# Performance work log

Hardware: AMD Instinct MI355X
Metric: run time of the kernel (lower is better)

## Reference

```python
import jax, jax.numpy as jnp
import numpy as np

EPS = 1e-12  # torch F.normalize default eps


def _l2norm(x):
    n = jnp.sqrt(jnp.sum(x * x, axis=-1, keepdims=True))
    return x / jnp.maximum(n, EPS)


def setup_inputs() -> dict:
    key = jax.random.key(0)
    ks = jax.random.split(key, 8)
    B, T, V = 4, 2048, 512
    C, H, NB = 512, 4, 64
    return {
        "x": jax.random.normal(ks[0], (B, T, V), dtype=jnp.float32),
        "basis": jax.random.normal(ks[1], (V, 2 * NB), dtype=jnp.float32),
        "shared_q_w": jax.random.normal(ks[2], (V, C), dtype=jnp.float32) * 0.02,
        "shared_k_w": jax.random.normal(ks[3], (V, C), dtype=jnp.float32) * 0.02,
        "v_coeffs": jax.random.normal(ks[4], (C, 2 * NB), dtype=jnp.float32) * 0.02,
        "o_coeffs": jax.random.normal(ks[5], (C, 2 * NB), dtype=jnp.float32) * 0.02,
        "decay_logits": jnp.linspace(1.0, 5.0, H, dtype=jnp.float32),
        "out_scale": jnp.float32(0.1),
    }


def reference(x, basis, shared_q_w, shared_k_w, v_coeffs, o_coeffs, decay_logits, out_scale):
    B, T, V = x.shape
    H = decay_logits.shape[0]
    C = shared_q_w.shape[1]
    D = C // H

    v_w = basis @ v_coeffs.T  # [V, C]
    o_w = basis @ o_coeffs.T  # [V, C]

    q = _l2norm(x @ shared_q_w)  # [B, T, C]
    k = _l2norm(x @ shared_k_w)
    v = x @ v_w

    # [B, H, T, D]
    q = q.reshape(B, T, H, D).transpose(0, 2, 1, 3)
    k = k.reshape(B, T, H, D).transpose(0, 2, 1, 3)
    v = v.reshape(B, T, H, D).transpose(0, 2, 1, 3)

    scores = jnp.einsum("bhqd,bhkd->bhqk", q, k)  # [B, H, T, T]

    decay = jax.nn.sigmoid(decay_logits)  # [H]
    pos = jnp.arange(T)
    diff = pos[None, :] - pos[:, None]  # diff[i, j] = j - i
    mask = (diff > 0).astype(scores.dtype)  # [T, T]
    expo = jnp.clip(diff.astype(jnp.float32) - 1.0, 0.0, None)  # [T, T]
    decay_w = (decay[:, None, None] ** expo[None]) * mask[None]  # [H, T, T]

    scores = scores * decay_w[None].astype(scores.dtype)
    retrieved = jnp.einsum("bhqk,bhkd->bhqd", scores, v)  # [B, H, T, D]
    retrieved = retrieved.transpose(0, 2, 1, 3).reshape(B, T, C)
    return retrieved @ o_w.T * out_scale  # [B, T, V]
```

## Files before the change

### kernel.cpp

```cpp
#include <hip/hip_runtime.h>
#include <hip/hip_bf16.h>

#define BB 4
#define TT 2048
#define VV 512
#define CC 512
#define HH 4
#define DD 128
#define NB2 128
#define NROWS (BB*TT)
#define QC 64
#define NCH (TT/QC)
#define SST 66
#define EPS 1e-12f

typedef __attribute__((ext_vector_type(8))) short bf16x8;
typedef __attribute__((ext_vector_type(4))) float f32x4;
typedef unsigned short u16;

__device__ __forceinline__ void gl_lds16(const void* g, void* l) {
    __builtin_amdgcn_global_load_lds(
        (const __attribute__((address_space(1))) unsigned int*)g,
        (__attribute__((address_space(3))) unsigned int*)l, 16, 0, 0);
}
__device__ __forceinline__ u16 f2bu(float x) {
    __hip_bfloat16 h = __float2bfloat16(x);
    return *reinterpret_cast<u16*>(&h);
}
__device__ __forceinline__ float bu2f(u16 u) {
    __hip_bfloat16 h = *reinterpret_cast<__hip_bfloat16*>(&u);
    return __bfloat162float(h);
}

#define PREP_CVT   4096
#define PREP_TR    512
#define PREP_CB    64
#define PREP_Z     16
__global__ __launch_bounds__(256) void prep_all(
    const float* __restrict__ x, const float* __restrict__ qw,
    const float* __restrict__ kw, const float* __restrict__ basis,
    const float* __restrict__ v_coeffs, const float* __restrict__ o_coeffs,
    const float* __restrict__ out_scale,
    u16* __restrict__ xb, u16* __restrict__ wq, u16* __restrict__ wk,
    u16* __restrict__ bab, u16* __restrict__ vcb, u16* __restrict__ ocb,
    float* __restrict__ norms)
{
    __shared__ float tile[32][33];
    const int bi = blockIdx.x, t = threadIdx.x;
    if (bi < PREP_CVT) {
        int i = bi * 256 + t;
        float4 v = ((const float4*)x)[i];
        u16 h[4] = {f2bu(v.x), f2bu(v.y), f2bu(v.z), f2bu(v.w)};
        ((uint2*)xb)[i] = *(uint2*)h;
    } else if (bi < PREP_CVT + PREP_TR) {
        int id = bi - PREP_CVT;
        const int z = id >> 8; id &= 255;
        const float* in = z ? kw : qw;
        u16* outT = z ? wk : wq;
        const int bx = (id & 15) * 32, by = (id >> 4) * 32;
        const int tx = t & 31, ty = t >> 5;
        #pragma unroll
        for (int r = 0; r < 32; r += 8)
            tile[ty + r][tx] = in[(size_t)(by + ty + r) * CC + bx + tx];
        __syncthreads();
        #pragma unroll
        for (int r = 0; r < 32; r += 8)
            outT[(size_t)(bx + ty + r) * VV + by + tx] = f2bu(tile[tx][ty + r]);
    } else if (bi < PREP_CVT + PREP_TR + 3 * PREP_CB) {
        int id = bi - PREP_CVT - PREP_TR;
        const int which = id / PREP_CB;
        int i = (id - which * PREP_CB) * 256 + t;
        const float* src = which == 0 ? basis : (which == 1 ? v_coeffs : o_coeffs);
        u16* dst = which == 0 ? bab : (which == 1 ? vcb : ocb);
        const float sc = which == 2 ? out_scale[0] : 1.f;
        float4 v = ((const float4*)src)[i];
        u16 h[4] = {f2bu(v.x * sc), f2bu(v.y * sc), f2bu(v.z * sc), f2bu(v.w * sc)};
        ((uint2*)dst)[i] = *(uint2*)h;
    } else {
        int idx = (bi - PREP_CVT - PREP_TR - 3 * PREP_CB) * 256 + t;
        ((float4*)norms)[idx] = make_float4(0.f, 0.f, 0.f, 0.f);
    }
}

template <bool BF16OUT, bool NORMS>
__device__ __forceinline__ void gemm_body(
    const u16* __restrict__ A, const u16* __restrict__ Bt,
    void* __restrict__ Cp, int M, int N, int K, int m0, int n0,
    u16* __restrict__ As, u16* __restrict__ Bs, float* __restrict__ normp)
{
    const int t = threadIdx.x;
    const int wave = t >> 6, lane = t & 63;
    const int qq = lane >> 4, l16 = lane & 15;
    const int wm = (wave >> 1) * 64, wn = (wave & 1) * 64;

    const int s0 = wave * 128 + lane, s1 = s0 + 64;
    const int r0_ = s0 >> 2, c0_ = ((s0 & 3) - (r0_ >> 1)) & 3;
    const int r1_ = s1 >> 2, c1_ = ((s1 & 3) - (r1_ >> 1)) & 3;
    const u16* ga0 = A  + (size_t)(m0 + r0_) * K + c0_ * 8;
    const u16* ga1 = A  + (size_t)(m0 + r1_) * K + c1_ * 8;
    const u16* gb0 = Bt + (size_t)(n0 + r0_) * K + c0_ * 8;
    const u16* gb1 = Bt + (size_t)(n0 + r1_) * K + c1_ * 8;
    const int lo0 = (wave * 128) * 8, lo1 = (wave * 128 + 64) * 8;

    gl_lds16(ga0, As + lo0);
    gl_lds16(ga1, As + lo1);
    gl_lds16(gb0, Bs + lo0);
    gl_lds16(gb1, Bs + lo1);

    f32x4 acc[4][4];
    #pragma unroll
    for (int i = 0; i < 4; ++i)
        #pragma unroll
        for (int j = 0; j < 4; ++j) acc[i][j] = (f32x4){0.f, 0.f, 0.f, 0.f};

    int ib = 0;
    for (int k0 = 0; k0 < K; k0 += 32, ib ^= 1) {
        __syncthreads();
        if (k0 + 32 < K) {
            const int off = (ib ^ 1) * 4096;
            gl_lds16(ga0 + k0 + 32, As + off + lo0);
            gl_lds16(ga1 + k0 + 32, As + off + lo1);
            gl_lds16(gb0 + k0 + 32, Bs + off + lo0);
            gl_lds16(gb1 + k0 + 32, Bs + off + lo1);
        }
        const u16* Ac = As + ib * 4096;
        const u16* Bc = Bs + ib * 4096;
        bf16x8 af[4], bfr[4];
        #pragma unroll
        for (int mt = 0; mt < 4; ++mt) {
            const int r = wm + mt * 16 + l16;
            af[mt] = *(const bf16x8*)&Ac[(r * 4 + ((qq + (r >> 1)) & 3)) * 8];
        }
        #pragma unroll
        for (int nt = 0; nt < 4; ++nt) {
            const int r = wn + nt * 16 + l16;
            bfr[nt] = *(const bf16x8*)&Bc[(r * 4 + ((qq + (r >> 1)) & 3)) * 8];
        }
        #pragma unroll
        for (int mt = 0; mt < 4; ++mt)
            #pragma unroll
            for (int nt = 0; nt < 4; ++nt)
                acc[mt][nt] = __builtin_amdgcn_mfma_f32_16x16x32_bf16(
                    af[mt], bfr[nt], acc[mt][nt], 0, 0, 0);
    }
    #pragma unroll
    for (int mt = 0; mt < 4; ++mt)
        #pragma unroll
        for (int r = 0; r < 4; ++r) {
            int grow = m0 + wm + mt * 16 + qq * 4 + r;
            #pragma unroll
            for (int nt = 0; nt < 4; ++nt) {
                int gcol = n0 + wn + nt * 16 + l16;
                if (BF16OUT)
                    ((u16*)Cp)[(size_t)grow * N + gcol] = f2bu(acc[mt][nt][r]);
                else
                    ((float*)Cp)[(size_t)grow * N + gcol] = acc[mt][nt][r];
            }
        }
    if (NORMS && normp) {
        #pragma unroll
        for (int mt = 0; mt < 4; ++mt)
            #pragma unroll
            for (int r = 0; r < 4; ++r) {
                float s = 0.f;
                #pragma unroll
                for (int nt = 0; nt < 4; ++nt) {
                    float v = acc[mt][nt][r];
                    s = fmaf(v, v, s);
                }
                s += __shfl_xor(s, 1, 64);
                s += __shfl_xor(s, 2, 64);
                s += __shfl_xor(s, 4, 64);
                s += __shfl_xor(s, 8, 64);
                if (l16 == 0)
                    atomicAdd(&normp[m0 + wm + mt * 16 + qq * 4 + r], s);
            }
    }
}

__global__ __launch_bounds__(256) void gemm_w(
    const u16* __restrict__ bab, const u16* __restrict__ vcb,
    const u16* __restrict__ ocb, u16* __restrict__ v_wT, u16* __restrict__ o_ws)
{
    __shared__ __align__(16) u16 As[8192];
    __shared__ __align__(16) u16 Bs[8192];
    const int sec = blockIdx.x >> 2;
    const u16* A  = sec ? bab : vcb;
    const u16* Bt = sec ? ocb : bab;
    u16* C = sec ? o_ws : v_wT;
    gemm_body<true, false>(A, Bt, C, 512, 512, NB2,
                           blockIdx.y * 128, (blockIdx.x & 3) * 128, As, Bs, nullptr);
}

__global__ __launch_bounds__(256) void gemm_qkv(
    const u16* __restrict__ xb, const u16* __restrict__ wcat,
    u16* __restrict__ qo, u16* __restrict__ ko, u16* __restrict__ vo,
    float* __restrict__ norms)
{
    __shared__ __align__(16) u16 As[8192];
    __shared__ __align__(16) u16 Bs[8192];
    const int sec = blockIdx.x >> 2;
    u16* outp = sec == 0 ? qo : (sec == 1 ? ko : vo);
    float* np = sec == 0 ? norms : (sec == 1 ? norms + NROWS : nullptr);
    gemm_body<true, true>(xb, wcat + (size_t)sec * VV * CC, outp,
                          NROWS, CC, VV, blockIdx.y * 128, (blockIdx.x & 3) * 128,
                          As, Bs, np);
}

__global__ __launch_bounds__(256) void gemm_out(
    const u16* __restrict__ Ab, const u16* __restrict__ Btb, float* __restrict__ C)
{
    __shared__ __align__(16) u16 As[8192];
    __shared__ __align__(16) u16 Bs[8192];
    gemm_body<false, false>(Ab, Btb, C, NROWS, VV, CC,
                            blockIdx.y * 128, blockIdx.x * 128, As, Bs, nullptr);
}

__global__ __launch_bounds__(256) void state_local(
    const u16* __restrict__ kb, const u16* __restrict__ vb,
    const float* __restrict__ norms_k, const float* __restrict__ dlog,
    u16* __restrict__ statesb)
{
    __shared__ float ksA[16][132];
    __shared__ float vsA[16][132];
    const int c  = blockIdx.x;
    const int bh = blockIdx.y;
    const int b = bh >> 2, h = bh & 3;
    const float lam = 1.f / (1.f + __expf(-dlog[h]));
    const float l2lam = log2f(lam);
    const int t = threadIdx.x;
    const int tx = t & 15, ty = t >> 4;
    const int row0 = b * TT + c * QC;
    const size_t gbase = (size_t)row0 * CC + h * DD;

    float acc[8][8] = {};

    for (int j0 = 0; j0 < QC; j0 += 16) {
        __syncthreads();
        {
            const int r = t >> 4, c8 = (t & 15) * 8;
            uint4 kraw = *(const uint4*)(kb + gbase + (size_t)(j0 + r) * CC + c8);
            uint4 vraw = *(const uint4*)(vb + gbase + (size_t)(j0 + r) * CC + c8);
            const u16* kp = (const u16*)&kraw;
            const u16* vp = (const u16*)&vraw;
            const float w = exp2f((float)(j0 + r) * l2lam);
            const float rk = 1.f / fmaxf(sqrtf(norms_k[row0 + j0 + r]), EPS);
            *(float4*)&ksA[r][c8]     = make_float4(bu2f(kp[0]) * rk, bu2f(kp[1]) * rk, bu2f(kp[2]) * rk, bu2f(kp[3]) * rk);
            *(float4*)&ksA[r][c8 + 4] = make_float4(bu2f(kp[4]) * rk, bu2f(kp[5]) * rk, bu2f(kp[6]) * rk, bu2f(kp[7]) * rk);
            *(float4*)&vsA[r][c8]     = make_float4(bu2f(vp[0]) * w, bu2f(vp[1]) * w, bu2f(vp[2]) * w, bu2f(vp[3]) * w);
            *(float4*)&vsA[r][c8 + 4] = make_float4(bu2f(vp[4]) * w, bu2f(vp[5]) * w, bu2f(vp[6]) * w, bu2f(vp[7]) * w);
        }
        __syncthreads();
        #pragma unroll
        for (int jj = 0; jj < 16; ++jj) {
            float4 va0 = *(const float4*)&vsA[jj][ty * 8];
            float4 va1 = *(const float4*)&vsA[jj][ty * 8 + 4];
            float4 ka0 = *(const float4*)&ksA[jj][tx * 8];
            float4 ka1 = *(const float4*)&ksA[jj][tx * 8 + 4];
            float vd[8] = {va0.x, va0.y, va0.z, va0.w, va1.x, va1.y, va1.z, va1.w};
            float ke[8] = {ka0.x, ka0.y, ka0.z, ka0.w, ka1.x, ka1.y, ka1.z, ka1.w};
            #pragma unroll
            for (int a = 0; a < 8; ++a)
                #pragma unroll
                for (int d = 0; d < 8; ++d)
                    acc[a][d] = fmaf(vd[a], ke[d], acc[a][d]);
        }
    }
    u16* so = statesb + ((size_t)(bh * NCH + c) << 14);
    #pragma unroll
    for (int a = 0; a < 8; ++a) {
        u16 h8[8];
        #pragma unroll
        for (int d = 0; d < 8; ++d) h8[d] = f2bu(acc[a][d]);
        *(uint4*)(so + (size_t)(ty * 8 + a) * DD + tx * 8) = *(uint4*)h8;
    }
}

__global__ __launch_bounds__(256) void state_combine(
    const float* __restrict__ dlog, u16* __restrict__ statesb)
{
    const int bh = blockIdx.x >> 3, part = blockIdx.x & 7;
    const int h = bh & 3;
    const float lam = 1.f / (1.f + __expf(-dlog[h]));
    const float lamQ = exp2f((float)QC * log2f(lam));
    const int t = threadIdx.x;
    float run[8] = {};
    uint4* pbase = (uint4*)(statesb + ((size_t)(bh * NCH) << 14)) + part * 256 + t;
    uint4 cur = pbase[(size_t)(NCH - 1) * 2048];
    for (int c = NCH - 1; c >= 0; --c) {
        uint4 nxt = cur;
        if (c) nxt = pbase[(size_t)(c - 1) * 2048];
        u16* hb = (u16*)&cur;
        uint4 outw;
        u16* ho = (u16*)&outw;
        #pragma unroll
        for (int i = 0; i < 8; ++i) {
            float tmp = bu2f(hb[i]);
            ho[i] = f2bu(run[i]);
            run[i] = fmaf(lamQ, run[i], tmp);
        }
        pbase[(size_t)c * 2048] = outw;
        cur = nxt;
    }
}

__global__ __launch_bounds__(256) void attention_fused(
    const u16* __restrict__ qb, const u16* __restrict__ kb,
    const u16* __restrict__ vb, const u16* __restrict__ statesb,
    const float* __restrict__ norms, const float* __restrict__ dlog,
    u16* __restrict__ retb)
{
    __shared__ __align__(16) u16 qs[QC][DD];
    __shared__ __align__(16) u16 ks[QC][DD];
    __shared__ __align__(16) u16 vsT[DD][SST];
    __shared__ __align__(16) u16 ss[QC][SST];
    __shared__ float rql[QC], rkl[QC];

    const int c = blockIdx.x, bh = blockIdx.y;
    const int b = bh >> 2, h = bh & 3;
    const float lam = 1.f / (1.f + __expf(-dlog[h]));
    const float l2lam = log2f(lam);
    const int t = threadIdx.x;
    const int row0 = b * TT + c * QC;
    const size_t base = (size_t)row0 * CC + h * DD;

    const int wave = t >> 6, lane = t & 63;
    const int quad = lane >> 4, l16 = lane & 15;
    const int r0 = wave * 16;

    {
        const int lrow = lane >> 4;
        const int lcol = (lane & 15) * 8;
        #pragma unroll
        for (int u = 0; u < 4; ++u) {
            const int r = wave * 16 + u * 4;
            gl_lds16(qb + base + (size_t)(r + lrow) * CC + lcol, &qs[r][0]);
            gl_lds16(kb + base + (size_t)(r + lrow) * CC + lcol, &ks[r][0]);
        }
    }
    if (t < QC)            rql[t]      = 1.f / fmaxf(sqrtf(norms[row0 + t]), EPS);
    else if (t < 2 * QC)   rkl[t - QC] = 1.f / fmaxf(sqrtf(norms[NROWS + row0 + t - QC]), EPS);
    {
        const int j2 = t & 31, d0 = (t >> 5) * 16;
        const u16* v0 = vb + base + (size_t)(2 * j2) * CC + d0;
        const u16* v1 = v0 + CC;
        uint4 a0 = *(const uint4*)v0;
        uint4 a1 = *(const uint4*)(v0 + 8);
        uint4 b0 = *(const uint4*)v1;
        uint4 b1 = *(const uint4*)(v1 + 8);
        const u16* ap0 = (const u16*)&a0; const u16* ap1 = (const u16*)&a1;
        const u16* bp0 = (const u16*)&b0; const u16* bp1 = (const u16*)&b1;
        #pragma unroll
        for (int i = 0; i < 8; ++i) {
            *(unsigned int*)&vsT[d0 + i][2 * j2] =
                (unsigned int)ap0[i] | ((unsigned int)bp0[i] << 16);
            *(unsigned int*)&vsT[d0 + 8 + i][2 * j2] =
                (unsigned int)ap1[i] | ((unsigned int)bp1[i] << 16);
        }
    }
    __syncthreads();

    bf16x8 aq[4];
    #pragma unroll
    for (int kq = 0; kq < 4; ++kq)
        aq[kq] = *(const bf16x8*)&qs[r0 + l16][kq * 32 + quad * 8];

    f32x4 accs[4];
    #pragma unroll
    for (int nt = 0; nt < 4; ++nt) accs[nt] = (f32x4){0.f, 0.f, 0.f, 0.f};
    #pragma unroll
    for (int nt = 0; nt < 4; ++nt)
        #pragma unroll
        for (int kq = 0; kq < 4; ++kq) {
            bf16x8 bk = *(const bf16x8*)&ks[nt * 16 + l16][kq * 32 + quad * 8];
            accs[nt] = __builtin_amdgcn_mfma_f32_16x16x32_bf16(aq[kq], bk, accs[nt], 0, 0, 0);
        }

    #pragma unroll
    for (int nt = 0; nt < 4; ++nt) {
        const int j = nt * 16 + l16;
        const float rkj = rkl[j];
        #pragma unroll
        for (int rr = 0; rr < 4; ++rr) {
            const int i = r0 + quad * 4 + rr;
            const int di = j - i;
            float p = (di > 0) ? accs[nt][rr] * exp2f((float)(di - 1) * l2lam) * rkj : 0.f;
            ss[i][j] = f2bu(p);
        }
    }

    const u16* sb = statesb + ((size_t)(bh * NCH + c) << 14);
    f32x4 accc[8];
    #pragma unroll
    for (int nt = 0; nt < 8; ++nt) accc[nt] = (f32x4){0.f, 0.f, 0.f, 0.f};
    #pragma unroll
    for (int nt = 0; nt < 8; ++nt)
        #pragma unroll
        for (int kq = 0; kq < 4; ++kq) {
            bf16x8 bs_ = *(const bf16x8*)(sb + (size_t)(nt * 16 + l16) * DD + kq * 32 + quad * 8);
            accc[nt] = __builtin_amdgcn_mfma_f32_16x16x32_bf16(aq[kq], bs_, accc[nt], 0, 0, 0);
        }

    bf16x8 ap[2];
    #pragma unroll
    for (int kj = 0; kj < 2; ++kj)
        ap[kj] = *(const bf16x8*)&ss[r0 + l16][kj * 32 + quad * 8];
    f32x4 accd[8];
    #pragma unroll
    for (int nt = 0; nt < 8; ++nt) accd[nt] = (f32x4){0.f, 0.f, 0.f, 0.f};
    #pragma unroll
    for (int nt = 0; nt < 8; ++nt)
        #pragma unroll
        for (int kj = 0; kj < 2; ++kj) {
            bf16x8 bv = *(const bf16x8*)&vsT[nt * 16 + l16][kj * 32 + quad * 8];
            accd[nt] = __builtin_amdgcn_mfma_f32_16x16x32_bf16(ap[kj], bv, accd[nt], 0, 0, 0);
        }

    u16* rb = retb + (size_t)row0 * CC + h * DD;
    #pragma unroll
    for (int rr = 0; rr < 4; ++rr) {
        const int ii = r0 + quad * 4 + rr;
        const float wrow = exp2f((float)(QC - 1 - ii) * l2lam);
        const float rq = rql[ii];
        #pragma unroll
        for (int nt = 0; nt < 8; ++nt) {
            float val = (accd[nt][rr] + wrow * accc[nt][rr]) * rq;
            rb[(size_t)ii * CC + nt * 16 + l16] = f2bu(val);
        }
    }
}

extern "C" void kernel_launch(void* const* d_in, const int* in_sizes, int n_in,
                              void* d_out, int out_size, void* d_ws, size_t ws_size,
                              hipStream_t stream) {
    const float* x         = (const float*)d_in[0];
    const float* basis     = (const float*)d_in[1];
    const float* qw        = (const float*)d_in[2];
    const float* kw        = (const float*)d_in[3];
    const float* v_coeffs  = (const float*)d_in[4];
    const float* o_coeffs  = (const float*)d_in[5];
    const float* dlog      = (const float*)d_in[6];
    const float* out_scale = (const float*)d_in[7];
    float* out             = (float*)d_out;

    u16* p = (u16*)d_ws;
    u16* qb      = p;
    u16* kb      = qb + (size_t)NROWS * CC;
    u16* vb      = kb + (size_t)NROWS * CC;
    u16* statesb = vb + (size_t)NROWS * CC;
    u16* xb      = statesb + (size_t)BB * HH * NCH * DD * DD;
    u16* retb    = xb;
    u16* wcat    = xb + (size_t)NROWS * CC;
    u16* o_ws    = wcat + 3 * (size_t)VV * CC;
    float* norms = (float*)(o_ws + (size_t)VV * CC);
    u16* bab     = (u16*)(norms + 2 * NROWS);
    u16* vcb     = bab + (size_t)VV * NB2;
    u16* ocb     = vcb + (size_t)VV * NB2;

    prep_all<<<PREP_CVT + PREP_TR + 3 * PREP_CB + PREP_Z, 256, 0, stream>>>(
        x, qw, kw, basis, v_coeffs, o_coeffs, out_scale,
        xb, wcat, wcat + (size_t)VV * CC, bab, vcb, ocb, norms);
    gemm_w<<<dim3(8, 4), 256, 0, stream>>>(bab, vcb, ocb,
                                           wcat + 2 * (size_t)VV * CC, o_ws);
    gemm_qkv<<<dim3(12, NROWS / 128), 256, 0, stream>>>(xb, wcat, qb, kb, vb, norms);
    state_local  <<<dim3(NCH, BB * HH), 256, 0, stream>>>(kb, vb, norms + NROWS,
                                                          dlog, statesb);
    state_combine<<<BB * HH * 8, 256, 0, stream>>>(dlog, statesb);
    attention_fused<<<dim3(NCH, BB * HH), 256, 0, stream>>>(qb, kb, vb, statesb,
                                                            norms, dlog, retb);
    gemm_out<<<dim3(CC / 128, NROWS / 128), 256, 0, stream>>>(retb, o_ws, out);
}
```

Before: 181.6 us.

## Use MFMA for chunk states, swizzle LDS in attention, shrink output GEMM tiles

The chunk-state kernel moves from scalar fp32 outer-product FMAs to bf16 MFMA over transposed K/V tiles in LDS, which adds bf16 rounding of the scaled inputs. The attention kernel now loads its state matrix through swizzled LDS reused from the Q/K buffer rather than reading it directly from global memory, and adds barriers to make that reuse safe. The output GEMM gets a dedicated 64x128 tile kernel, doubling the block count to improve occupancy across CUs. These changes target the scalar-compute bottleneck in state_local and the poorly-coalesced global state reads.

```diff
diff --git a/kernel.cpp b/kernel.cpp
--- a/kernel.cpp
+++ b/kernel.cpp
@@ -207,13 +207,75 @@
                           As, Bs, np);
 }
 
-__global__ __launch_bounds__(256) void gemm_out(
-    const u16* __restrict__ Ab, const u16* __restrict__ Btb, float* __restrict__ C)
-{
-    __shared__ __align__(16) u16 As[8192];
+__global__ __launch_bounds__(256) void gemm_out64(
+    const u16* __restrict__ A, const u16* __restrict__ Bt, float* __restrict__ C)
+{
+    __shared__ __align__(16) u16 As[4096];
     __shared__ __align__(16) u16 Bs[8192];
-    gemm_body<false, false>(Ab, Btb, C, NROWS, VV, CC,
-                            blockIdx.y * 128, blockIdx.x * 128, As, Bs, nullptr);
+    const int t = threadIdx.x;
+    const int wave = t >> 6, lane = t & 63;
+    const int qq = lane >> 4, l16 = lane & 15;
+    const int m0 = blockIdx.y * 64, n0 = blockIdx.x * 128;
+    const int wm = (wave >> 1) * 32, wn = (wave & 1) * 64;
+    const int N = VV, K = CC;
+
+    const int sA = wave * 64 + lane;
+    const int rA = sA >> 2, cA = ((sA & 3) - (rA >> 1)) & 3;
+    const int sB0 = wave * 128 + lane, sB1 = sB0 + 64;
+    const int rB0 = sB0 >> 2, cB0 = ((sB0 & 3) - (rB0 >> 1)) & 3;
+    const int rB1 = sB1 >> 2, cB1 = ((sB1 & 3) - (rB1 >> 1)) & 3;
+    const u16* ga  = A  + (size_t)(m0 + rA) * K + cA * 8;
+    const u16* gb0 = Bt + (size_t)(n0 + rB0) * K + cB0 * 8;
+    const u16* gb1 = Bt + (size_t)(n0 + rB1) * K + cB1 * 8;
+    const int loA = wave * 512, loB0 = wave * 1024, loB1 = wave * 1024 + 512;
+
+    gl_lds16(ga, As + loA);
+    gl_lds16(gb0, Bs + loB0);
+    gl_lds16(gb1, Bs + loB1);
+
+    f32x4 acc[2][4];
+    #pragma unroll
+    for (int i = 0; i < 2; ++i)
+        #pragma unroll
+        for (int j = 0; j < 4; ++j) acc[i][j] = (f32x4){0.f, 0.f, 0.f, 0.f};
+
+    int ib = 0;
+    for (int k0 = 0; k0 < K; k0 += 32, ib ^= 1) {
+        __syncthreads();
+        if (k0 + 32 < K) {
+            gl_lds16(ga + k0 + 32,  As + (ib ^ 1) * 2048 + loA);
+            gl_lds16(gb0 + k0 + 32, Bs + (ib ^ 1) * 4096 + loB0);
+            gl_lds16(gb1 + k0 + 32, Bs + (ib ^ 1) * 4096 + loB1);
+        }
+        const u16* Ac = As + ib * 2048;
+        const u16* Bc = Bs + ib * 4096;
+        bf16x8 af[2], bfr[4];
+        #pragma unroll
+        for (int mt = 0; mt < 2; ++mt) {
+            const int r = wm + mt * 16 + l16;
+            af[mt] = *(const bf16x8*)&Ac[(r * 4 + ((qq + (r >> 1)) & 3)) * 8];
+        }
+        #pragma unroll
+        for (int nt = 0; nt < 4; ++nt) {
+            const int r = wn + nt * 16 + l16;
+            bfr[nt] = *(const bf16x8*)&Bc[(r * 4 + ((qq + (r >> 1)) & 3)) * 8];
+        }
+        #pragma unroll
+        for (int mt = 0; mt < 2; ++mt)
+            #pragma unroll
+            for (int nt = 0; nt < 4; ++nt)
+                acc[mt][nt] = __builtin_amdgcn_mfma_f32_16x16x32_bf16(
+                    af[mt], bfr[nt], acc[mt][nt], 0, 0, 0);
+    }
+    #pragma unroll
+    for (int mt = 0; mt < 2; ++mt)
+        #pragma unroll
+        for (int r = 0; r < 4; ++r) {
+            int grow = m0 + wm + mt * 16 + qq * 4 + r;
+            #pragma unroll
+            for (int nt = 0; nt < 4; ++nt)
+                C[(size_t)grow * N + n0 + wn + nt * 16 + l16] = acc[mt][nt][r];
+        }
 }
 
 __global__ __launch_bounds__(256) void state_local(
@@ -221,59 +283,77 @@
     const float* __restrict__ norms_k, const float* __restrict__ dlog,
     u16* __restrict__ statesb)
 {
-    __shared__ float ksA[16][132];
-    __shared__ float vsA[16][132];
-    const int c  = blockIdx.x;
-    const int bh = blockIdx.y;
+    __shared__ __align__(16) u16 vT[DD][SST];
+    __shared__ __align__(16) u16 kT[DD][SST];
+    const int c = blockIdx.x, bh = blockIdx.y;
     const int b = bh >> 2, h = bh & 3;
     const float lam = 1.f / (1.f + __expf(-dlog[h]));
     const float l2lam = log2f(lam);
     const int t = threadIdx.x;
-    const int tx = t & 15, ty = t >> 4;
     const int row0 = b * TT + c * QC;
     const size_t gbase = (size_t)row0 * CC + h * DD;
 
-    float acc[8][8] = {};
-
-    for (int j0 = 0; j0 < QC; j0 += 16) {
-        __syncthreads();
-        {
-            const int r = t >> 4, c8 = (t & 15) * 8;
-            uint4 kraw = *(const uint4*)(kb + gbase + (size_t)(j0 + r) * CC + c8);
-            uint4 vraw = *(const uint4*)(vb + gbase + (size_t)(j0 + r) * CC + c8);
-            const u16* kp = (const u16*)&kraw;
-            const u16* vp = (const u16*)&vraw;
-            const float w = exp2f((float)(j0 + r) * l2lam);
-            const float rk = 1.f / fmaxf(sqrtf(norms_k[row0 + j0 + r]), EPS);
-            *(float4*)&ksA[r][c8]     = make_float4(bu2f(kp[0]) * rk, bu2f(kp[1]) * rk, bu2f(kp[2]) * rk, bu2f(kp[3]) * rk);
-            *(float4*)&ksA[r][c8 + 4] = make_float4(bu2f(kp[4]) * rk, bu2f(kp[5]) * rk, bu2f(kp[6]) * rk, bu2f(kp[7]) * rk);
-            *(float4*)&vsA[r][c8]     = make_float4(bu2f(vp[0]) * w, bu2f(vp[1]) * w, bu2f(vp[2]) * w, bu2f(vp[3]) * w);
-            *(float4*)&vsA[r][c8 + 4] = make_float4(bu2f(vp[4]) * w, bu2f(vp[5]) * w, bu2f(vp[6]) * w, bu2f(vp[7]) * w);
-        }
-        __syncthreads();
-        #pragma unroll
-        for (int jj = 0; jj < 16; ++jj) {
-            float4 va0 = *(const float4*)&vsA[jj][ty * 8];
-            float4 va1 = *(const float4*)&vsA[jj][ty * 8 + 4];
-            float4 ka0 = *(const float4*)&ksA[jj][tx * 8];
-            float4 ka1 = *(const float4*)&ksA[jj][tx * 8 + 4];
-            float vd[8] = {va0.x, va0.y, va0.z, va0.w, va1.x, va1.y, va1.z, va1.w};
-            float ke[8] = {ka0.x, ka0.y, ka0.z, ka0.w, ka1.x, ka1.y, ka1.z, ka1.w};
-            #pragma unroll
-            for (int a = 0; a < 8; ++a)
-                #pragma unroll
-                for (int d = 0; d < 8; ++d)
-                    acc[a][d] = fmaf(vd[a], ke[d], acc[a][d]);
+    {
+        const int j2 = t & 31, d0 = (t >> 5) * 16;
+        const int jj0 = 2 * j2, jj1 = jj0 + 1;
+        const float w0 = exp2f((float)jj0 * l2lam);
+        const float w1 = exp2f((float)jj1 * l2lam);
+        const float rk0 = 1.f / fmaxf(sqrtf(norms_k[row0 + jj0]), EPS);
+        const float rk1 = 1.f / fmaxf(sqrtf(norms_k[row0 + jj1]), EPS);
+        u16 k0a[16], k1a[16], v0a[16], v1a[16];
+        const u16* k0p = kb + gbase + (size_t)jj0 * CC + d0;
+        const u16* k1p = kb + gbase + (size_t)jj1 * CC + d0;
+        const u16* v0p = vb + gbase + (size_t)jj0 * CC + d0;
+        const u16* v1p = vb + gbase + (size_t)jj1 * CC + d0;
+        *(uint4*)&k0a[0] = *(const uint4*)k0p; *(uint4*)&k0a[8] = *(const uint4*)(k0p + 8);
+        *(uint4*)&k1a[0] = *(const uint4*)k1p; *(uint4*)&k1a[8] = *(const uint4*)(k1p + 8);
+        *(uint4*)&v0a[0] = *(const uint4*)v0p; *(uint4*)&v0a[8] = *(const uint4*)(v0p + 8);
+        *(uint4*)&v1a[0] = *(const uint4*)v1p; *(uint4*)&v1a[8] = *(const uint4*)(v1p + 8);
+        #pragma unroll
+        for (int i = 0; i < 16; ++i) {
+            unsigned int kw = (unsigned int)f2bu(bu2f(k0a[i]) * rk0)
+                            | ((unsigned int)f2bu(bu2f(k1a[i]) * rk1) << 16);
+            *(unsigned int*)&kT[d0 + i][jj0] = kw;
+            unsigned int vw = (unsigned int)f2bu(bu2f(v0a[i]) * w0)
+                            | ((unsigned int)f2bu(bu2f(v1a[i]) * w1) << 16);
+            *(unsigned int*)&vT[d0 + i][jj0] = vw;
+        }
+    }
+    __syncthreads();
+
+    const int wave = t >> 6, lane = t & 63;
+    const int quad = lane >> 4, l16 = lane & 15;
+    f32x4 acc[2][8];
+    #pragma unroll
+    for (int i = 0; i < 2; ++i)
+        #pragma unroll
+        for (int j = 0; j < 8; ++j) acc[i][j] = (f32x4){0.f, 0.f, 0.f, 0.f};
+
+    #pragma unroll
+    for (int s = 0; s < 2; ++s) {
+        bf16x8 af[2];
+        #pragma unroll
+        for (int mt = 0; mt < 2; ++mt)
+            af[mt] = *(const bf16x8*)&vT[wave * 32 + mt * 16 + l16][s * 32 + quad * 8];
+        #pragma unroll
+        for (int nt = 0; nt < 8; ++nt) {
+            bf16x8 bk = *(const bf16x8*)&kT[nt * 16 + l16][s * 32 + quad * 8];
+            #pragma unroll
+            for (int mt = 0; mt < 2; ++mt)
+                acc[mt][nt] = __builtin_amdgcn_mfma_f32_16x16x32_bf16(
+                    af[mt], bk, acc[mt][nt], 0, 0, 0);
         }
     }
     u16* so = statesb + ((size_t)(bh * NCH + c) << 14);
     #pragma unroll
-    for (int a = 0; a < 8; ++a) {
-        u16 h8[8];
-        #pragma unroll
-        for (int d = 0; d < 8; ++d) h8[d] = f2bu(acc[a][d]);
-        *(uint4*)(so + (size_t)(ty * 8 + a) * DD + tx * 8) = *(uint4*)h8;
-    }
+    for (int mt = 0; mt < 2; ++mt)
+        #pragma unroll
+        for (int rr = 0; rr < 4; ++rr) {
+            const int d = wave * 32 + mt * 16 + quad * 4 + rr;
+            #pragma unroll
+            for (int nt = 0; nt < 8; ++nt)
+                so[(size_t)d * DD + nt * 16 + l16] = f2bu(acc[mt][nt][rr]);
+        }
 }
 
 __global__ __launch_bounds__(256) void state_combine(
@@ -310,8 +390,7 @@
     const float* __restrict__ norms, const float* __restrict__ dlog,
     u16* __restrict__ retb)
 {
-    __shared__ __align__(16) u16 qs[QC][DD];
-    __shared__ __align__(16) u16 ks[QC][DD];
+    __shared__ __align__(16) u16 qks[2 * QC * DD];
     __shared__ __align__(16) u16 vsT[DD][SST];
     __shared__ __align__(16) u16 ss[QC][SST];
     __shared__ float rql[QC], rkl[QC];
@@ -329,13 +408,14 @@
     const int r0 = wave * 16;
 
     {
-        const int lrow = lane >> 4;
-        const int lcol = (lane & 15) * 8;
+        const int lrow = lane >> 4, cch = lane & 15;
         #pragma unroll
         for (int u = 0; u < 4; ++u) {
-            const int r = wave * 16 + u * 4;
-            gl_lds16(qb + base + (size_t)(r + lrow) * CC + lcol, &qs[r][0]);
-            gl_lds16(kb + base + (size_t)(r + lrow) * CC + lcol, &ks[r][0]);
+            const int R = wave * 16 + u * 4;
+            const int gr = R + lrow;
+            const int cq = (cch - gr) & 15;
+            gl_lds16(qb + base + (size_t)gr * CC + cq * 8, &qks[R * DD]);
+            gl_lds16(kb + base + (size_t)gr * CC + cq * 8, &qks[(QC + R) * DD]);
         }
     }
     if (t < QC)            rql[t]      = 1.f / fmaxf(sqrtf(norms[row0 + t]), EPS);
@@ -362,8 +442,10 @@
 
     bf16x8 aq[4];
     #pragma unroll
-    for (int kq = 0; kq < 4; ++kq)
-        aq[kq] = *(const bf16x8*)&qs[r0 + l16][kq * 32 + quad * 8];
+    for (int kq = 0; kq < 4; ++kq) {
+        const int r = r0 + l16;
+        aq[kq] = *(const bf16x8*)&qks[r * DD + ((kq * 4 + quad + r) & 15) * 8];
+    }
 
     f32x4 accs[4];
     #pragma unroll
@@ -372,7 +454,8 @@
     for (int nt = 0; nt < 4; ++nt)
         #pragma unroll
         for (int kq = 0; kq < 4; ++kq) {
-            bf16x8 bk = *(const bf16x8*)&ks[nt * 16 + l16][kq * 32 + quad * 8];
+            const int rk_ = nt * 16 + l16;
+            bf16x8 bk = *(const bf16x8*)&qks[(QC + rk_) * DD + ((kq * 4 + quad + rk_) & 15) * 8];
             accs[nt] = __builtin_amdgcn_mfma_f32_16x16x32_bf16(aq[kq], bk, accs[nt], 0, 0, 0);
         }
 
@@ -388,19 +471,19 @@
             ss[i][j] = f2bu(p);
         }
     }
+    __syncthreads();
 
     const u16* sb = statesb + ((size_t)(bh * NCH + c) << 14);
-    f32x4 accc[8];
-    #pragma unroll
-    for (int nt = 0; nt < 8; ++nt) accc[nt] = (f32x4){0.f, 0.f, 0.f, 0.f};
-    #pragma unroll
-    for (int nt = 0; nt < 8; ++nt)
-        #pragma unroll
-        for (int kq = 0; kq < 4; ++kq) {
-            bf16x8 bs_ = *(const bf16x8*)(sb + (size_t)(nt * 16 + l16) * DD + kq * 32 + quad * 8);
-            accc[nt] = __builtin_amdgcn_mfma_f32_16x16x32_bf16(aq[kq], bs_, accc[nt], 0, 0, 0);
-        }
-
+    {
+        const int drow = lane >> 4, cch = lane & 15;
+        #pragma unroll
+        for (int u = 0; u < 8; ++u) {
+            const int D = wave * 32 + u * 4;
+            const int gd = D + drow;
+            const int cq = (cch - gd) & 15;
+            gl_lds16(sb + (size_t)gd * DD + cq * 8, &qks[D * DD]);
+        }
+    }
     bf16x8 ap[2];
     #pragma unroll
     for (int kj = 0; kj < 2; ++kj)
@@ -414,6 +497,19 @@
         for (int kj = 0; kj < 2; ++kj) {
             bf16x8 bv = *(const bf16x8*)&vsT[nt * 16 + l16][kj * 32 + quad * 8];
             accd[nt] = __builtin_amdgcn_mfma_f32_16x16x32_bf16(ap[kj], bv, accd[nt], 0, 0, 0);
+        }
+    __syncthreads();
+
+    f32x4 accc[8];
+    #pragma unroll
+    for (int nt = 0; nt < 8; ++nt) accc[nt] = (f32x4){0.f, 0.f, 0.f, 0.f};
+    #pragma unroll
+    for (int nt = 0; nt < 8; ++nt)
+        #pragma unroll
+        for (int kq = 0; kq < 4; ++kq) {
+            const int d = nt * 16 + l16;
+            bf16x8 bs_ = *(const bf16x8*)&qks[d * DD + ((kq * 4 + quad + d) & 15) * 8];
+            accc[nt] = __builtin_amdgcn_mfma_f32_16x16x32_bf16(aq[kq], bs_, accc[nt], 0, 0, 0);
         }
 
     u16* rb = retb + (size_t)row0 * CC + h * DD;
@@ -468,5 +564,5 @@
     state_combine<<<BB * HH * 8, 256, 0, stream>>>(dlog, statesb);
     attention_fused<<<dim3(NCH, BB * HH), 256, 0, stream>>>(qb, kb, vb, statesb,
                                                             norms, dlog, retb);
-    gemm_out<<<dim3(CC / 128, NROWS / 128), 256, 0, stream>>>(retb, o_ws, out);
-}
+    gemm_out64<<<dim3(VV / 128, NROWS / 64), 256, 0, stream>>>(retb, o_ws, out);
+}
```

New measurement: 168.9 us. 1.08x faster.
